# Optimization experiments

Hardware: AMD Instinct MI355X
Metric: run time of the kernel (lower is better)

## Reference

```python
import jax, jax.numpy as jnp
import numpy as np

N_EVENTS = 4_000_000
T_WINDOW = 100.0


def setup_inputs() -> dict:
    key = jax.random.key(0)
    k_ts, = jax.random.split(key, 1)
    # sorted event times in [0, T)
    ts = jnp.sort(jax.random.uniform(k_ts, (N_EVENTS,), dtype=jnp.float32) * T_WINDOW)
    mu = jnp.float32(0.5)
    log_alpha = jnp.log(jnp.float32(0.5))   # alpha = 0.5 (branching ratio < 1)
    log_beta = jnp.log(jnp.float32(2.0))    # beta = 2.0
    return {"ts": ts, "mu": mu, "log_alpha": log_alpha, "log_beta": log_beta, "T": 100}


def reference(ts, mu, log_alpha, log_beta, T):
    """Log-likelihood of a univariate exponential-kernel Hawkes process.

    Equivalent to UnivariateHawkesProcess.likelihood(ts, T, log=True,
    num_integration_points=0, analy_kernel=True), but the O(N^2) per-event
    Python loop is replaced by a stable O(N) exclusive cumulative logsumexp:
        sum_{j<i} exp(-beta (t_i - t_j)) = exp(logcumsumexp(beta t)_{i-1} - beta t_i)
    """
    alpha = jnp.exp(log_alpha)
    beta = jnp.exp(log_beta)
    Tf = jnp.asarray(T, dtype=ts.dtype)

    b_ts = beta * ts                               # [N]
    incl = jax.lax.cumlogsumexp(b_ts)              # inclusive running logsumexp
    excl = jnp.concatenate([jnp.full((1,), -jnp.inf, dtype=b_ts.dtype), incl[:-1]])
    decay_sum = jnp.exp(excl - b_ts)               # sum_{j<i} exp(-beta(t_i - t_j))
    intensities = mu + alpha * beta * decay_sum    # lambda(t_i | history)
    positive_ll = jnp.sum(jnp.log(intensities))

    # analytic compensator: mu*T + sum_i alpha/beta * (1 - exp(-beta (T - t_i)))
    integral = mu * Tf + jnp.sum((alpha / beta) * (1.0 - jnp.exp(-beta * (Tf - ts))))
    return positive_ll - integral
```

## Files before the change

### kernel.cpp

```cpp
#include <hip/hip_runtime.h>

#define SEG 64
#define TPB 256

struct DA { float d, a; };

__device__ __forceinline__ DA da_compose(DA f, DA g) {
    DA r; r.d = f.d * g.d; r.a = fmaf(f.a, g.d, g.a); return r;
}

__global__ void __launch_bounds__(TPB) hawkes_phase1(
    const float* __restrict__ ts, const float* __restrict__ lb_p,
    const int* __restrict__ T_p, int N, int NSEG,
    DA* __restrict__ segDA, DA* __restrict__ blkDA)
{
    const float beta = __expf(*lb_p);
    const int tid = threadIdx.x;
    const int g = blockIdx.x * TPB + tid;

    DA my; my.d = 1.f; my.a = 0.f;
    if (g < NSEG) {
        const int start = g * SEG;
        const int end = min(start + SEG, N);
        const float Tf = (float)(*T_p);
        const float rnext = (end < N) ? ts[end] : Tf;
        float R, t0, tprev;
        if (end == start + SEG) {
            const float4* p = (const float4*)(ts + start);
            float4 v = p[0];
            t0 = v.x; tprev = t0; R = 1.f;
            { float e = __expf(-beta * (v.y - tprev)); R = fmaf(R, e, 1.f); tprev = v.y; }
            { float e = __expf(-beta * (v.z - tprev)); R = fmaf(R, e, 1.f); tprev = v.z; }
            { float e = __expf(-beta * (v.w - tprev)); R = fmaf(R, e, 1.f); tprev = v.w; }
            #pragma unroll
            for (int q = 1; q < SEG / 4; ++q) {
                float4 w4 = p[q];
                { float e = __expf(-beta * (w4.x - tprev)); R = fmaf(R, e, 1.f); tprev = w4.x; }
                { float e = __expf(-beta * (w4.y - tprev)); R = fmaf(R, e, 1.f); tprev = w4.y; }
                { float e = __expf(-beta * (w4.z - tprev)); R = fmaf(R, e, 1.f); tprev = w4.z; }
                { float e = __expf(-beta * (w4.w - tprev)); R = fmaf(R, e, 1.f); tprev = w4.w; }
            }
        } else {
            t0 = ts[start]; tprev = t0; R = 1.f;
            for (int j = start + 1; j < end; ++j) {
                float t = ts[j];
                float e = __expf(-beta * (t - tprev)); R = fmaf(R, e, 1.f); tprev = t;
            }
        }
        my.a = R * __expf(-beta * (rnext - tprev));
        my.d = __expf(-beta * (rnext - t0));
        segDA[g] = my;
    }

    __shared__ DA lds[TPB];
    lds[tid] = my;
    __syncthreads();
    #pragma unroll
    for (int s = 1; s < TPB; s <<= 1) {
        if ((tid & (2 * s - 1)) == 0) lds[tid] = da_compose(lds[tid], lds[tid + s]);
        __syncthreads();
    }
    if (tid == 0) blkDA[blockIdx.x] = lds[0];
}

__global__ void __launch_bounds__(TPB) hawkes_phase2(
    const DA* __restrict__ blkDA, int NB,
    float* __restrict__ blkCarry, float* __restrict__ stats ,
    double* __restrict__ acc)
{
    const int tid = threadIdx.x;
    if (tid == 0) *acc = 0.0;

    const int K2 = (NB + TPB - 1) / TPB;
    const int b0 = min(tid * K2, NB);
    const int b1 = min(b0 + K2, NB);

    DA comp; comp.d = 1.f; comp.a = 0.f;
    for (int b = b0; b < b1; ++b) comp = da_compose(comp, blkDA[b]);

    const int lane = tid & 63, wave = tid >> 6;
    DA inc = comp;
    #pragma unroll
    for (int off = 1; off < 64; off <<= 1) {
        DA up; up.d = __shfl_up(inc.d, off); up.a = __shfl_up(inc.a, off);
        if (lane >= off) inc = da_compose(up, inc);
    }
    __shared__ DA waveAgg[TPB / 64];
    if (lane == 63) waveAgg[wave] = inc;
    __syncthreads();
    DA pre; pre.d = 1.f; pre.a = 0.f;
    for (int w = 0; w < wave; ++w) pre = da_compose(pre, waveAgg[w]);
    DA lexcl; lexcl.d = __shfl_up(inc.d, 1); lexcl.a = __shfl_up(inc.a, 1);
    if (lane == 0) { lexcl.d = 1.f; lexcl.a = 0.f; }
    DA excl = da_compose(pre, lexcl);

    float c = excl.a;
    for (int b = b0; b < b1; ++b) {
        blkCarry[b] = c;
        DA x = blkDA[b];
        c = fmaf(c, x.d, x.a);
    }
    if (b0 < NB && b1 == NB) stats[0] = c;
}

__global__ void __launch_bounds__(TPB) hawkes_phase3(
    const float* __restrict__ ts,
    const float* __restrict__ mu_p, const float* __restrict__ la_p,
    const float* __restrict__ lb_p, int N, int NSEG,
    const DA* __restrict__ segDA, const float* __restrict__ blkCarry,
    double* __restrict__ acc)
{
    const float mu = *mu_p;
    const float beta = __expf(*lb_p);
    const float ab = __expf(*la_p) * beta;
    const int tid = threadIdx.x;
    const int g = blockIdx.x * TPB + tid;
    const int lane = tid & 63, wave = tid >> 6;

    DA my; my.d = 1.f; my.a = 0.f;
    if (g < NSEG) my = segDA[g];

    DA inc = my;
    #pragma unroll
    for (int off = 1; off < 64; off <<= 1) {
        DA up; up.d = __shfl_up(inc.d, off); up.a = __shfl_up(inc.a, off);
        if (lane >= off) inc = da_compose(up, inc);
    }
    __shared__ DA waveAgg[TPB / 64];
    if (lane == 63) waveAgg[wave] = inc;
    __syncthreads();
    DA pre; pre.d = 1.f; pre.a = 0.f;
    for (int w = 0; w < wave; ++w) pre = da_compose(pre, waveAgg[w]);
    DA lexcl; lexcl.d = __shfl_up(inc.d, 1); lexcl.a = __shfl_up(inc.a, 1);
    if (lane == 0) { lexcl.d = 1.f; lexcl.a = 0.f; }
    DA excl = da_compose(pre, lexcl);

    const float bc = blkCarry[blockIdx.x];
    float S = fmaf(bc, excl.d, excl.a);

    float lsum = 0.f;
    if (g < NSEG) {
        const int start = g * SEG;
        const int end = min(start + SEG, N);
        if (end == start + SEG) {
            const float4* p = (const float4*)(ts + start);
            float4 v = p[0];
            float tprev = v.x;
            lsum += __logf(fmaf(ab, S, mu));
#define HSTEP(tt) { float e = __expf(-beta * ((tt) - tprev)); S = fmaf(S, e, e); \
                    lsum += __logf(fmaf(ab, S, mu)); tprev = (tt); }
            HSTEP(v.y); HSTEP(v.z); HSTEP(v.w);
            #pragma unroll
            for (int q = 1; q < SEG / 4; ++q) {
                float4 w4 = p[q];
                HSTEP(w4.x); HSTEP(w4.y); HSTEP(w4.z); HSTEP(w4.w);
            }
#undef HSTEP
        } else {
            float tprev = ts[start];
            lsum += __logf(fmaf(ab, S, mu));
            for (int j = start + 1; j < end; ++j) {
                float t = ts[j];
                float e = __expf(-beta * (t - tprev));
                S = fmaf(S, e, e);
                lsum += __logf(fmaf(ab, S, mu));
                tprev = t;
            }
        }
    }

    #pragma unroll
    for (int off = 32; off > 0; off >>= 1) lsum += __shfl_down(lsum, off);
    __shared__ float wsum[TPB / 64];
    if (lane == 0) wsum[wave] = lsum;
    __syncthreads();
    if (tid == 0) {
        float tot = 0.f;
        #pragma unroll
        for (int w = 0; w < TPB / 64; ++w) tot += wsum[w];
        atomicAdd(acc, (double)tot);
    }
}

__global__ void hawkes_phase4(
    const double* __restrict__ acc, const float* __restrict__ stats,
    const float* __restrict__ mu_p, const float* __restrict__ la_p,
    const float* __restrict__ lb_p, const int* __restrict__ T_p,
    int N, float* __restrict__ out)
{
    const float mu = *mu_p;
    const float alpha = __expf(*la_p);
    const float beta = __expf(*lb_p);
    const float Tf = (float)(*T_p);
    const float integral = mu * Tf + (alpha / beta) * ((float)N - stats[0]);
    out[0] = (float)(*acc) - integral;
}

extern "C" void kernel_launch(void* const* d_in, const int* in_sizes, int n_in,
                              void* d_out, int out_size, void* d_ws, size_t ws_size,
                              hipStream_t stream) {
    const float* ts = (const float*)d_in[0];
    const float* mu = (const float*)d_in[1];
    const float* la = (const float*)d_in[2];
    const float* lb = (const float*)d_in[3];
    const int*   T  = (const int*)d_in[4];
    const int N = in_sizes[0];
    const int NSEG = (N + SEG - 1) / SEG;
    const int NB = (NSEG + TPB - 1) / TPB;

    char* w = (char*)d_ws;
    double* acc      = (double*)w;
    float*  stats    = (float*)(w + 8);
    DA*     segDA    = (DA*)(w + 16);
    DA*     blkDA    = (DA*)(w + 16 + (size_t)NSEG * sizeof(DA));
    float*  blkCarry = (float*)(w + 16 + (size_t)(NSEG + NB) * sizeof(DA));

    hawkes_phase1<<<NB, TPB, 0, stream>>>(ts, lb, T, N, NSEG, segDA, blkDA);
    hawkes_phase2<<<1, TPB, 0, stream>>>(blkDA, NB, blkCarry, stats, acc);
    hawkes_phase3<<<NB, TPB, 0, stream>>>(ts, mu, la, lb, N, NSEG, segDA, blkCarry, acc);
    hawkes_phase4<<<1, 1, 0, stream>>>(acc, stats, mu, la, lb, T, N, (float*)d_out);
}
```

Before: 82.33 us.

## Fuse four scan phases into one cooperative kernel with register-cached decays

Replaces the four-kernel pipeline (segment aggregate, block-carry scan, local rescan, finalize) with a single cooperative kernel that uses grid-wide syncs between phases. Each thread keeps its 64 decay factors in registers, so the second pass needs neither the re-read of ts nor the exp recompute, and segDA no longer goes to global memory. The global atomic is replaced by per-block partial sums that block 0 reduces at the end. The design relies on all NB blocks (about 245 here) being co-resident for the grid sync. It also adds register pressure from the 64-float array and the cost of grid barriers.

```diff
diff --git a/kernel.cpp b/kernel.cpp
--- a/kernel.cpp
+++ b/kernel.cpp
@@ -1,4 +1,7 @@
 #include <hip/hip_runtime.h>
+#include <hip/hip_cooperative_groups.h>
+
+namespace cg = cooperative_groups;
 
 #define SEG 64
 #define TPB 256
@@ -9,77 +12,69 @@
     DA r; r.d = f.d * g.d; r.a = fmaf(f.a, g.d, g.a); return r;
 }
 
-__global__ void __launch_bounds__(TPB) hawkes_phase1(
-    const float* __restrict__ ts, const float* __restrict__ lb_p,
-    const int* __restrict__ T_p, int N, int NSEG,
-    DA* __restrict__ segDA, DA* __restrict__ blkDA)
+__global__ void __launch_bounds__(TPB, 1) hawkes_fused(
+    const float* __restrict__ ts,
+    const float* __restrict__ mu_p, const float* __restrict__ la_p,
+    const float* __restrict__ lb_p, const int* __restrict__ T_p,
+    int N, int NSEG, int NB,
+    DA* __restrict__ blkDA, float* __restrict__ blkCarry,
+    double* __restrict__ blkSum, float* __restrict__ stats,
+    float* __restrict__ out)
 {
-    const float beta = __expf(*lb_p);
-    const int tid = threadIdx.x;
-    const int g = blockIdx.x * TPB + tid;
-
+    cg::grid_group grid = cg::this_grid();
+    const float beta  = __expf(*lb_p);
+    const float mu    = *mu_p;
+    const float alpha = __expf(*la_p);
+    const float ab    = alpha * beta;
+    const float Tf    = (float)(*T_p);
+    const int tid  = threadIdx.x;
+    const int g    = blockIdx.x * TPB + tid;
+    const int lane = tid & 63, wave = tid >> 6;
+
+    float e[SEG];
     DA my; my.d = 1.f; my.a = 0.f;
+    bool full = false;
+    const int start = g * SEG;
+    const int end   = (g < NSEG) ? min(start + SEG, N) : start;
     if (g < NSEG) {
-        const int start = g * SEG;
-        const int end = min(start + SEG, N);
-        const float Tf = (float)(*T_p);
+        full = (end == start + SEG);
         const float rnext = (end < N) ? ts[end] : Tf;
-        float R, t0, tprev;
-        if (end == start + SEG) {
+        float R = 1.f, t0, tprev;
+        if (full) {
             const float4* p = (const float4*)(ts + start);
             float4 v = p[0];
-            t0 = v.x; tprev = t0; R = 1.f;
-            { float e = __expf(-beta * (v.y - tprev)); R = fmaf(R, e, 1.f); tprev = v.y; }
-            { float e = __expf(-beta * (v.z - tprev)); R = fmaf(R, e, 1.f); tprev = v.z; }
-            { float e = __expf(-beta * (v.w - tprev)); R = fmaf(R, e, 1.f); tprev = v.w; }
+            t0 = v.x;
+            e[1] = __expf(-beta * (v.y - v.x));
+            e[2] = __expf(-beta * (v.z - v.y));
+            e[3] = __expf(-beta * (v.w - v.z));
+            R = fmaf(R, e[1], 1.f); R = fmaf(R, e[2], 1.f); R = fmaf(R, e[3], 1.f);
+            tprev = v.w;
             #pragma unroll
             for (int q = 1; q < SEG / 4; ++q) {
                 float4 w4 = p[q];
-                { float e = __expf(-beta * (w4.x - tprev)); R = fmaf(R, e, 1.f); tprev = w4.x; }
-                { float e = __expf(-beta * (w4.y - tprev)); R = fmaf(R, e, 1.f); tprev = w4.y; }
-                { float e = __expf(-beta * (w4.z - tprev)); R = fmaf(R, e, 1.f); tprev = w4.z; }
-                { float e = __expf(-beta * (w4.w - tprev)); R = fmaf(R, e, 1.f); tprev = w4.w; }
+                e[4*q+0] = __expf(-beta * (w4.x - tprev));
+                e[4*q+1] = __expf(-beta * (w4.y - w4.x));
+                e[4*q+2] = __expf(-beta * (w4.z - w4.y));
+                e[4*q+3] = __expf(-beta * (w4.w - w4.z));
+                R = fmaf(R, e[4*q+0], 1.f);
+                R = fmaf(R, e[4*q+1], 1.f);
+                R = fmaf(R, e[4*q+2], 1.f);
+                R = fmaf(R, e[4*q+3], 1.f);
+                tprev = w4.w;
             }
         } else {
-            t0 = ts[start]; tprev = t0; R = 1.f;
+            t0 = ts[start]; tprev = t0;
             for (int j = start + 1; j < end; ++j) {
                 float t = ts[j];
-                float e = __expf(-beta * (t - tprev)); R = fmaf(R, e, 1.f); tprev = t;
+                float ee = __expf(-beta * (t - tprev));
+                R = fmaf(R, ee, 1.f); tprev = t;
             }
         }
         my.a = R * __expf(-beta * (rnext - tprev));
         my.d = __expf(-beta * (rnext - t0));
-        segDA[g] = my;
-    }
-
-    __shared__ DA lds[TPB];
-    lds[tid] = my;
-    __syncthreads();
-    #pragma unroll
-    for (int s = 1; s < TPB; s <<= 1) {
-        if ((tid & (2 * s - 1)) == 0) lds[tid] = da_compose(lds[tid], lds[tid + s]);
-        __syncthreads();
-    }
-    if (tid == 0) blkDA[blockIdx.x] = lds[0];
-}
-
-__global__ void __launch_bounds__(TPB) hawkes_phase2(
-    const DA* __restrict__ blkDA, int NB,
-    float* __restrict__ blkCarry, float* __restrict__ stats ,
-    double* __restrict__ acc)
-{
-    const int tid = threadIdx.x;
-    if (tid == 0) *acc = 0.0;
-
-    const int K2 = (NB + TPB - 1) / TPB;
-    const int b0 = min(tid * K2, NB);
-    const int b1 = min(b0 + K2, NB);
-
-    DA comp; comp.d = 1.f; comp.a = 0.f;
-    for (int b = b0; b < b1; ++b) comp = da_compose(comp, blkDA[b]);
-
-    const int lane = tid & 63, wave = tid >> 6;
-    DA inc = comp;
+    }
+
+    DA inc = my;
     #pragma unroll
     for (int off = 1; off < 64; off <<= 1) {
         DA up; up.d = __shfl_up(inc.d, off); up.a = __shfl_up(inc.a, off);
@@ -93,82 +88,69 @@
     DA lexcl; lexcl.d = __shfl_up(inc.d, 1); lexcl.a = __shfl_up(inc.a, 1);
     if (lane == 0) { lexcl.d = 1.f; lexcl.a = 0.f; }
     DA excl = da_compose(pre, lexcl);
-
-    float c = excl.a;
-    for (int b = b0; b < b1; ++b) {
-        blkCarry[b] = c;
-        DA x = blkDA[b];
-        c = fmaf(c, x.d, x.a);
-    }
-    if (b0 < NB && b1 == NB) stats[0] = c;
-}
-
-__global__ void __launch_bounds__(TPB) hawkes_phase3(
-    const float* __restrict__ ts,
-    const float* __restrict__ mu_p, const float* __restrict__ la_p,
-    const float* __restrict__ lb_p, int N, int NSEG,
-    const DA* __restrict__ segDA, const float* __restrict__ blkCarry,
-    double* __restrict__ acc)
-{
-    const float mu = *mu_p;
-    const float beta = __expf(*lb_p);
-    const float ab = __expf(*la_p) * beta;
-    const int tid = threadIdx.x;
-    const int g = blockIdx.x * TPB + tid;
-    const int lane = tid & 63, wave = tid >> 6;
-
-    DA my; my.d = 1.f; my.a = 0.f;
-    if (g < NSEG) my = segDA[g];
-
-    DA inc = my;
-    #pragma unroll
-    for (int off = 1; off < 64; off <<= 1) {
-        DA up; up.d = __shfl_up(inc.d, off); up.a = __shfl_up(inc.a, off);
-        if (lane >= off) inc = da_compose(up, inc);
-    }
-    __shared__ DA waveAgg[TPB / 64];
-    if (lane == 63) waveAgg[wave] = inc;
-    __syncthreads();
-    DA pre; pre.d = 1.f; pre.a = 0.f;
-    for (int w = 0; w < wave; ++w) pre = da_compose(pre, waveAgg[w]);
-    DA lexcl; lexcl.d = __shfl_up(inc.d, 1); lexcl.a = __shfl_up(inc.a, 1);
-    if (lane == 0) { lexcl.d = 1.f; lexcl.a = 0.f; }
-    DA excl = da_compose(pre, lexcl);
+    if (tid == TPB - 1) {
+        DA agg = da_compose(pre, inc);
+        blkDA[blockIdx.x] = agg;
+    }
+    __threadfence();
+    grid.sync();
+
+    if (blockIdx.x == 0) {
+        const int K2 = (NB + TPB - 1) / TPB;
+        const int b0 = min(tid * K2, NB);
+        const int b1 = min(b0 + K2, NB);
+        DA comp; comp.d = 1.f; comp.a = 0.f;
+        for (int b = b0; b < b1; ++b) comp = da_compose(comp, blkDA[b]);
+        DA inc2 = comp;
+        #pragma unroll
+        for (int off = 1; off < 64; off <<= 1) {
+            DA up; up.d = __shfl_up(inc2.d, off); up.a = __shfl_up(inc2.a, off);
+            if (lane >= off) inc2 = da_compose(up, inc2);
+        }
+        __shared__ DA waveAgg2[TPB / 64];
+        if (lane == 63) waveAgg2[wave] = inc2;
+        __syncthreads();
+        DA pre2; pre2.d = 1.f; pre2.a = 0.f;
+        for (int w = 0; w < wave; ++w) pre2 = da_compose(pre2, waveAgg2[w]);
+        DA lex2; lex2.d = __shfl_up(inc2.d, 1); lex2.a = __shfl_up(inc2.a, 1);
+        if (lane == 0) { lex2.d = 1.f; lex2.a = 0.f; }
+        DA ex2 = da_compose(pre2, lex2);
+        float c = ex2.a;
+        for (int b = b0; b < b1; ++b) {
+            blkCarry[b] = c;
+            DA x = blkDA[b];
+            c = fmaf(c, x.d, x.a);
+        }
+        if (b0 < NB && b1 == NB) stats[0] = c;
+        __threadfence();
+    }
+    grid.sync();
 
     const float bc = blkCarry[blockIdx.x];
     float S = fmaf(bc, excl.d, excl.a);
-
-    float lsum = 0.f;
+    float lsum0 = 0.f, lsum1 = 0.f;
     if (g < NSEG) {
-        const int start = g * SEG;
-        const int end = min(start + SEG, N);
-        if (end == start + SEG) {
-            const float4* p = (const float4*)(ts + start);
-            float4 v = p[0];
-            float tprev = v.x;
-            lsum += __logf(fmaf(ab, S, mu));
-#define HSTEP(tt) { float e = __expf(-beta * ((tt) - tprev)); S = fmaf(S, e, e); \
-                    lsum += __logf(fmaf(ab, S, mu)); tprev = (tt); }
-            HSTEP(v.y); HSTEP(v.z); HSTEP(v.w);
+        if (full) {
+            lsum0 += __logf(fmaf(ab, S, mu));
             #pragma unroll
-            for (int q = 1; q < SEG / 4; ++q) {
-                float4 w4 = p[q];
-                HSTEP(w4.x); HSTEP(w4.y); HSTEP(w4.z); HSTEP(w4.w);
-            }
-#undef HSTEP
+            for (int k = 1; k < SEG - 1; k += 2) {
+                { float ek = e[k];   S = fmaf(S, ek, ek); lsum1 += __logf(fmaf(ab, S, mu)); }
+                { float ek = e[k+1]; S = fmaf(S, ek, ek); lsum0 += __logf(fmaf(ab, S, mu)); }
+            }
+            { float ek = e[SEG-1]; S = fmaf(S, ek, ek); lsum1 += __logf(fmaf(ab, S, mu)); }
         } else {
             float tprev = ts[start];
-            lsum += __logf(fmaf(ab, S, mu));
+            lsum0 += __logf(fmaf(ab, S, mu));
             for (int j = start + 1; j < end; ++j) {
                 float t = ts[j];
-                float e = __expf(-beta * (t - tprev));
-                S = fmaf(S, e, e);
-                lsum += __logf(fmaf(ab, S, mu));
+                float ee = __expf(-beta * (t - tprev));
+                S = fmaf(S, ee, ee);
+                lsum0 += __logf(fmaf(ab, S, mu));
                 tprev = t;
             }
         }
     }
-
+    float lsum = lsum0 + lsum1;
     #pragma unroll
     for (int off = 32; off > 0; off >>= 1) lsum += __shfl_down(lsum, off);
     __shared__ float wsum[TPB / 64];
@@ -178,22 +160,26 @@
         float tot = 0.f;
         #pragma unroll
         for (int w = 0; w < TPB / 64; ++w) tot += wsum[w];
-        atomicAdd(acc, (double)tot);
-    }
-}
-
-__global__ void hawkes_phase4(
-    const double* __restrict__ acc, const float* __restrict__ stats,
-    const float* __restrict__ mu_p, const float* __restrict__ la_p,
-    const float* __restrict__ lb_p, const int* __restrict__ T_p,
-    int N, float* __restrict__ out)
-{
-    const float mu = *mu_p;
-    const float alpha = __expf(*la_p);
-    const float beta = __expf(*lb_p);
-    const float Tf = (float)(*T_p);
-    const float integral = mu * Tf + (alpha / beta) * ((float)N - stats[0]);
-    out[0] = (float)(*acc) - integral;
+        blkSum[blockIdx.x] = (double)tot;
+    }
+    __threadfence();
+    grid.sync();
+
+    if (blockIdx.x == 0) {
+        double v = (tid < NB) ? blkSum[tid] : 0.0;
+        #pragma unroll
+        for (int off = 32; off > 0; off >>= 1) v += __shfl_down(v, off);
+        __shared__ double dsum[TPB / 64];
+        if (lane == 0) dsum[wave] = v;
+        __syncthreads();
+        if (tid == 0) {
+            double tot = 0.0;
+            #pragma unroll
+            for (int w = 0; w < TPB / 64; ++w) tot += dsum[w];
+            const float integral = mu * Tf + (alpha / beta) * ((float)N - stats[0]);
+            out[0] = (float)(tot - (double)integral);
+        }
+    }
 }
 
 extern "C" void kernel_launch(void* const* d_in, const int* in_sizes, int n_in,
@@ -204,19 +190,21 @@
     const float* la = (const float*)d_in[2];
     const float* lb = (const float*)d_in[3];
     const int*   T  = (const int*)d_in[4];
-    const int N = in_sizes[0];
-    const int NSEG = (N + SEG - 1) / SEG;
-    const int NB = (NSEG + TPB - 1) / TPB;
+    int N = in_sizes[0];
+    int NSEG = (N + SEG - 1) / SEG;
+    int NB = (NSEG + TPB - 1) / TPB;
 
     char* w = (char*)d_ws;
-    double* acc      = (double*)w;
-    float*  stats    = (float*)(w + 8);
-    DA*     segDA    = (DA*)(w + 16);
-    DA*     blkDA    = (DA*)(w + 16 + (size_t)NSEG * sizeof(DA));
-    float*  blkCarry = (float*)(w + 16 + (size_t)(NSEG + NB) * sizeof(DA));
-
-    hawkes_phase1<<<NB, TPB, 0, stream>>>(ts, lb, T, N, NSEG, segDA, blkDA);
-    hawkes_phase2<<<1, TPB, 0, stream>>>(blkDA, NB, blkCarry, stats, acc);
-    hawkes_phase3<<<NB, TPB, 0, stream>>>(ts, mu, la, lb, N, NSEG, segDA, blkCarry, acc);
-    hawkes_phase4<<<1, 1, 0, stream>>>(acc, stats, mu, la, lb, T, N, (float*)d_out);
+    double* blkSum   = (double*)w;
+    DA*     blkDA    = (DA*)(w + (size_t)NB * 8);
+    float*  blkCarry = (float*)(w + (size_t)NB * 16);
+    float*  stats    = (float*)(w + (size_t)NB * 20);
+    float*  out      = (float*)d_out;
+
+    void* args[] = { (void*)&ts, (void*)&mu, (void*)&la, (void*)&lb, (void*)&T,
+                     (void*)&N, (void*)&NSEG, (void*)&NB,
+                     (void*)&blkDA, (void*)&blkCarry, (void*)&blkSum,
+                     (void*)&stats, (void*)&out };
+    hipLaunchCooperativeKernel((const void*)hawkes_fused, dim3(NB), dim3(TPB),
+                               args, 0, stream);
 }
```

New measurement: 202.5 us. 146% more time.

## Fuse four-phase scan into two kernels with redundant block-carry scan and ticket finish

Applied to the files above, without the earlier changes.

Reduces the pipeline from four launches to two. Each block in the second kernel redundantly scans all block aggregates to get its own carry, and the last block to arrive (via an atomic ticket) writes the final result. The per-segment DA array is dropped, and the second kernel recomputes segment summaries from ts, keeping the exponentials in registers. The segment length falls from 64 to 16, giving four times more blocks for occupancy. In exchange, the exp work is duplicated across both kernels and every block rereads the full block-aggregate array.

```diff
diff --git a/kernel.cpp b/kernel.cpp
--- a/kernel.cpp
+++ b/kernel.cpp
@@ -1,6 +1,6 @@
 #include <hip/hip_runtime.h>
 
-#define SEG 64
+#define SEG 16
 #define TPB 256
 
 struct DA { float d, a; };
@@ -9,160 +9,191 @@
     DA r; r.d = f.d * g.d; r.a = fmaf(f.a, g.d, g.a); return r;
 }
 
-__global__ void __launch_bounds__(TPB) hawkes_phase1(
+__global__ void __launch_bounds__(TPB) hawkes_k1(
     const float* __restrict__ ts, const float* __restrict__ lb_p,
     const int* __restrict__ T_p, int N, int NSEG,
-    DA* __restrict__ segDA, DA* __restrict__ blkDA)
+    DA* __restrict__ blkDA, double* __restrict__ acc, unsigned* __restrict__ ticket)
 {
     const float beta = __expf(*lb_p);
+    const float Tf = (float)(*T_p);
     const int tid = threadIdx.x;
     const int g = blockIdx.x * TPB + tid;
+    const int lane = tid & 63, wave = tid >> 6;
+
+    if (blockIdx.x == 0 && tid == 0) { *acc = 0.0; *ticket = 0u; }
 
     DA my; my.d = 1.f; my.a = 0.f;
     if (g < NSEG) {
         const int start = g * SEG;
         const int end = min(start + SEG, N);
-        const float Tf = (float)(*T_p);
-        const float rnext = (end < N) ? ts[end] : Tf;
-        float R, t0, tprev;
+        float R = 1.f, t0, tlast;
         if (end == start + SEG) {
             const float4* p = (const float4*)(ts + start);
-            float4 v = p[0];
-            t0 = v.x; tprev = t0; R = 1.f;
-            { float e = __expf(-beta * (v.y - tprev)); R = fmaf(R, e, 1.f); tprev = v.y; }
-            { float e = __expf(-beta * (v.z - tprev)); R = fmaf(R, e, 1.f); tprev = v.z; }
-            { float e = __expf(-beta * (v.w - tprev)); R = fmaf(R, e, 1.f); tprev = v.w; }
-            #pragma unroll
-            for (int q = 1; q < SEG / 4; ++q) {
-                float4 w4 = p[q];
-                { float e = __expf(-beta * (w4.x - tprev)); R = fmaf(R, e, 1.f); tprev = w4.x; }
-                { float e = __expf(-beta * (w4.y - tprev)); R = fmaf(R, e, 1.f); tprev = w4.y; }
-                { float e = __expf(-beta * (w4.z - tprev)); R = fmaf(R, e, 1.f); tprev = w4.z; }
-                { float e = __expf(-beta * (w4.w - tprev)); R = fmaf(R, e, 1.f); tprev = w4.w; }
-            }
+            float4 a = p[0], b = p[1], c = p[2], d = p[3];
+            t0 = a.x;
+            float tp = a.x;
+#define K1S(tt) { R = fmaf(R, __expf(-beta * ((tt) - tp)), 1.f); tp = (tt); }
+            K1S(a.y) K1S(a.z) K1S(a.w)
+            K1S(b.x) K1S(b.y) K1S(b.z) K1S(b.w)
+            K1S(c.x) K1S(c.y) K1S(c.z) K1S(c.w)
+            K1S(d.x) K1S(d.y) K1S(d.z) K1S(d.w)
+#undef K1S
+            tlast = d.w;
         } else {
-            t0 = ts[start]; tprev = t0; R = 1.f;
+            t0 = ts[start]; tlast = t0;
             for (int j = start + 1; j < end; ++j) {
                 float t = ts[j];
-                float e = __expf(-beta * (t - tprev)); R = fmaf(R, e, 1.f); tprev = t;
-            }
-        }
-        my.a = R * __expf(-beta * (rnext - tprev));
+                R = fmaf(R, __expf(-beta * (t - tlast)), 1.f); tlast = t;
+            }
+        }
+        const float rnext = (end < N) ? ts[end] : Tf;
+        my.a = R * __expf(-beta * (rnext - tlast));
         my.d = __expf(-beta * (rnext - t0));
-        segDA[g] = my;
-    }
-
-    __shared__ DA lds[TPB];
-    lds[tid] = my;
-    __syncthreads();
-    #pragma unroll
-    for (int s = 1; s < TPB; s <<= 1) {
-        if ((tid & (2 * s - 1)) == 0) lds[tid] = da_compose(lds[tid], lds[tid + s]);
-        __syncthreads();
-    }
-    if (tid == 0) blkDA[blockIdx.x] = lds[0];
-}
-
-__global__ void __launch_bounds__(TPB) hawkes_phase2(
-    const DA* __restrict__ blkDA, int NB,
-    float* __restrict__ blkCarry, float* __restrict__ stats ,
-    double* __restrict__ acc)
-{
-    const int tid = threadIdx.x;
-    if (tid == 0) *acc = 0.0;
-
-    const int K2 = (NB + TPB - 1) / TPB;
-    const int b0 = min(tid * K2, NB);
-    const int b1 = min(b0 + K2, NB);
-
-    DA comp; comp.d = 1.f; comp.a = 0.f;
-    for (int b = b0; b < b1; ++b) comp = da_compose(comp, blkDA[b]);
-
-    const int lane = tid & 63, wave = tid >> 6;
-    DA inc = comp;
+    }
+
+    DA inc = my;
     #pragma unroll
     for (int off = 1; off < 64; off <<= 1) {
         DA up; up.d = __shfl_up(inc.d, off); up.a = __shfl_up(inc.a, off);
         if (lane >= off) inc = da_compose(up, inc);
     }
-    __shared__ DA waveAgg[TPB / 64];
-    if (lane == 63) waveAgg[wave] = inc;
+    __shared__ DA wagg[TPB / 64];
+    if (lane == 63) wagg[wave] = inc;
+    __syncthreads();
+    if (tid == 0) {
+        DA aggr = wagg[0];
+        #pragma unroll
+        for (int w = 1; w < TPB / 64; ++w) aggr = da_compose(aggr, wagg[w]);
+        blkDA[blockIdx.x] = aggr;
+    }
+}
+
+__global__ void __launch_bounds__(TPB) hawkes_k2(
+    const float* __restrict__ ts,
+    const float* __restrict__ mu_p, const float* __restrict__ la_p,
+    const float* __restrict__ lb_p, const int* __restrict__ T_p,
+    int N, int NSEG, int NB,
+    const DA* __restrict__ blkDA, double* __restrict__ acc,
+    unsigned* __restrict__ ticket, float* __restrict__ out)
+{
+    const float beta  = __expf(*lb_p);
+    const float mu    = *mu_p;
+    const float alpha = __expf(*la_p);
+    const float ab    = alpha * beta;
+    const float Tf    = (float)(*T_p);
+    const int tid = threadIdx.x;
+    const int g = blockIdx.x * TPB + tid;
+    const int lane = tid & 63, wave = tid >> 6;
+
+    float e[SEG];
+    DA my; my.d = 1.f; my.a = 0.f;
+    bool full = false;
+    const int start = g * SEG;
+    const int end = (g < NSEG) ? min(start + SEG, N) : start;
+    if (g < NSEG) {
+        full = (end == start + SEG);
+        float R = 1.f, t0, tlast;
+        if (full) {
+            const float4* p = (const float4*)(ts + start);
+            float4 a = p[0], b = p[1], c = p[2], d = p[3];
+            t0 = a.x;
+            e[1]  = __expf(-beta * (a.y - a.x));
+            e[2]  = __expf(-beta * (a.z - a.y));
+            e[3]  = __expf(-beta * (a.w - a.z));
+            e[4]  = __expf(-beta * (b.x - a.w));
+            e[5]  = __expf(-beta * (b.y - b.x));
+            e[6]  = __expf(-beta * (b.z - b.y));
+            e[7]  = __expf(-beta * (b.w - b.z));
+            e[8]  = __expf(-beta * (c.x - b.w));
+            e[9]  = __expf(-beta * (c.y - c.x));
+            e[10] = __expf(-beta * (c.z - c.y));
+            e[11] = __expf(-beta * (c.w - c.z));
+            e[12] = __expf(-beta * (d.x - c.w));
+            e[13] = __expf(-beta * (d.y - d.x));
+            e[14] = __expf(-beta * (d.z - d.y));
+            e[15] = __expf(-beta * (d.w - d.z));
+            #pragma unroll
+            for (int k = 1; k < SEG; ++k) R = fmaf(R, e[k], 1.f);
+            tlast = d.w;
+        } else {
+            t0 = ts[start]; tlast = t0;
+            for (int j = start + 1; j < end; ++j) {
+                float t = ts[j];
+                R = fmaf(R, __expf(-beta * (t - tlast)), 1.f); tlast = t;
+            }
+        }
+        const float rnext = (end < N) ? ts[end] : Tf;
+        my.a = R * __expf(-beta * (rnext - tlast));
+        my.d = __expf(-beta * (rnext - t0));
+    }
+
+    DA inc = my;
+    #pragma unroll
+    for (int off = 1; off < 64; off <<= 1) {
+        DA up; up.d = __shfl_up(inc.d, off); up.a = __shfl_up(inc.a, off);
+        if (lane >= off) inc = da_compose(up, inc);
+    }
+    __shared__ DA wagg[TPB / 64];
+    if (lane == 63) wagg[wave] = inc;
     __syncthreads();
     DA pre; pre.d = 1.f; pre.a = 0.f;
-    for (int w = 0; w < wave; ++w) pre = da_compose(pre, waveAgg[w]);
+    for (int w = 0; w < wave; ++w) pre = da_compose(pre, wagg[w]);
     DA lexcl; lexcl.d = __shfl_up(inc.d, 1); lexcl.a = __shfl_up(inc.a, 1);
     if (lane == 0) { lexcl.d = 1.f; lexcl.a = 0.f; }
     DA excl = da_compose(pre, lexcl);
 
-    float c = excl.a;
-    for (int b = b0; b < b1; ++b) {
-        blkCarry[b] = c;
-        DA x = blkDA[b];
-        c = fmaf(c, x.d, x.a);
-    }
-    if (b0 < NB && b1 == NB) stats[0] = c;
-}
-
-__global__ void __launch_bounds__(TPB) hawkes_phase3(
-    const float* __restrict__ ts,
-    const float* __restrict__ mu_p, const float* __restrict__ la_p,
-    const float* __restrict__ lb_p, int N, int NSEG,
-    const DA* __restrict__ segDA, const float* __restrict__ blkCarry,
-    double* __restrict__ acc)
-{
-    const float mu = *mu_p;
-    const float beta = __expf(*lb_p);
-    const float ab = __expf(*la_p) * beta;
-    const int tid = threadIdx.x;
-    const int g = blockIdx.x * TPB + tid;
-    const int lane = tid & 63, wave = tid >> 6;
-
-    DA my; my.d = 1.f; my.a = 0.f;
-    if (g < NSEG) my = segDA[g];
-
-    DA inc = my;
+    const int CH = (NB + TPB - 1) / TPB;
+    DA comp; comp.d = 1.f; comp.a = 0.f;
+    for (int j = 0; j < CH; ++j) {
+        const int idx = tid * CH + j;
+        if (idx < NB) comp = da_compose(comp, blkDA[idx]);
+    }
+    DA inc2 = comp;
     #pragma unroll
     for (int off = 1; off < 64; off <<= 1) {
-        DA up; up.d = __shfl_up(inc.d, off); up.a = __shfl_up(inc.a, off);
-        if (lane >= off) inc = da_compose(up, inc);
-    }
-    __shared__ DA waveAgg[TPB / 64];
-    if (lane == 63) waveAgg[wave] = inc;
-    __syncthreads();
-    DA pre; pre.d = 1.f; pre.a = 0.f;
-    for (int w = 0; w < wave; ++w) pre = da_compose(pre, waveAgg[w]);
-    DA lexcl; lexcl.d = __shfl_up(inc.d, 1); lexcl.a = __shfl_up(inc.a, 1);
-    if (lane == 0) { lexcl.d = 1.f; lexcl.a = 0.f; }
-    DA excl = da_compose(pre, lexcl);
-
-    const float bc = blkCarry[blockIdx.x];
-    float S = fmaf(bc, excl.d, excl.a);
-
+        DA up; up.d = __shfl_up(inc2.d, off); up.a = __shfl_up(inc2.a, off);
+        if (lane >= off) inc2 = da_compose(up, inc2);
+    }
+    __shared__ DA wagg2[TPB / 64];
+    if (lane == 63) wagg2[wave] = inc2;
+    __syncthreads();
+    DA pre2; pre2.d = 1.f; pre2.a = 0.f;
+    for (int w = 0; w < wave; ++w) pre2 = da_compose(pre2, wagg2[w]);
+    DA lex2; lex2.d = __shfl_up(inc2.d, 1); lex2.a = __shfl_up(inc2.a, 1);
+    if (lane == 0) { lex2.d = 1.f; lex2.a = 0.f; }
+    DA chunkExcl = da_compose(pre2, lex2);
+
+    __shared__ DA exclArr[TPB];
+    __shared__ DA totalSh;
+    exclArr[tid] = chunkExcl;
+    if (tid == TPB - 1) totalSh = da_compose(pre2, inc2);
+    __syncthreads();
+
+    const int b = blockIdx.x;
+    const int c0 = b / CH, pp = b - c0 * CH;
+    DA E = exclArr[c0];
+    for (int j = 0; j < pp; ++j) E = da_compose(E, blkDA[c0 * CH + j]);
+    const float carry = E.a;
+    const float S_T = totalSh.a;
+
+    float S = fmaf(carry, excl.d, excl.a);
     float lsum = 0.f;
     if (g < NSEG) {
-        const int start = g * SEG;
-        const int end = min(start + SEG, N);
-        if (end == start + SEG) {
-            const float4* p = (const float4*)(ts + start);
-            float4 v = p[0];
-            float tprev = v.x;
+        if (full) {
             lsum += __logf(fmaf(ab, S, mu));
-#define HSTEP(tt) { float e = __expf(-beta * ((tt) - tprev)); S = fmaf(S, e, e); \
-                    lsum += __logf(fmaf(ab, S, mu)); tprev = (tt); }
-            HSTEP(v.y); HSTEP(v.z); HSTEP(v.w);
             #pragma unroll
-            for (int q = 1; q < SEG / 4; ++q) {
-                float4 w4 = p[q];
-                HSTEP(w4.x); HSTEP(w4.y); HSTEP(w4.z); HSTEP(w4.w);
-            }
-#undef HSTEP
+            for (int k = 1; k < SEG; ++k) {
+                float ek = e[k];
+                S = fmaf(S, ek, ek);
+                lsum += __logf(fmaf(ab, S, mu));
+            }
         } else {
             float tprev = ts[start];
             lsum += __logf(fmaf(ab, S, mu));
             for (int j = start + 1; j < end; ++j) {
                 float t = ts[j];
-                float e = __expf(-beta * (t - tprev));
-                S = fmaf(S, e, e);
+                float ee = __expf(-beta * (t - tprev));
+                S = fmaf(S, ee, ee);
                 lsum += __logf(fmaf(ab, S, mu));
                 tprev = t;
             }
@@ -179,21 +210,15 @@
         #pragma unroll
         for (int w = 0; w < TPB / 64; ++w) tot += wsum[w];
         atomicAdd(acc, (double)tot);
-    }
-}
-
-__global__ void hawkes_phase4(
-    const double* __restrict__ acc, const float* __restrict__ stats,
-    const float* __restrict__ mu_p, const float* __restrict__ la_p,
-    const float* __restrict__ lb_p, const int* __restrict__ T_p,
-    int N, float* __restrict__ out)
-{
-    const float mu = *mu_p;
-    const float alpha = __expf(*la_p);
-    const float beta = __expf(*lb_p);
-    const float Tf = (float)(*T_p);
-    const float integral = mu * Tf + (alpha / beta) * ((float)N - stats[0]);
-    out[0] = (float)(*acc) - integral;
+        __threadfence();
+        unsigned old = atomicAdd(ticket, 1u);
+        if (old == (unsigned)(NB - 1)) {
+            __threadfence();
+            double tt = atomicAdd(acc, 0.0);
+            const float integral = mu * Tf + (alpha / beta) * ((float)N - S_T);
+            out[0] = (float)(tt - (double)integral);
+        }
+    }
 }
 
 extern "C" void kernel_launch(void* const* d_in, const int* in_sizes, int n_in,
@@ -209,14 +234,11 @@
     const int NB = (NSEG + TPB - 1) / TPB;
 
     char* w = (char*)d_ws;
-    double* acc      = (double*)w;
-    float*  stats    = (float*)(w + 8);
-    DA*     segDA    = (DA*)(w + 16);
-    DA*     blkDA    = (DA*)(w + 16 + (size_t)NSEG * sizeof(DA));
-    float*  blkCarry = (float*)(w + 16 + (size_t)(NSEG + NB) * sizeof(DA));
-
-    hawkes_phase1<<<NB, TPB, 0, stream>>>(ts, lb, T, N, NSEG, segDA, blkDA);
-    hawkes_phase2<<<1, TPB, 0, stream>>>(blkDA, NB, blkCarry, stats, acc);
-    hawkes_phase3<<<NB, TPB, 0, stream>>>(ts, mu, la, lb, N, NSEG, segDA, blkCarry, acc);
-    hawkes_phase4<<<1, 1, 0, stream>>>(acc, stats, mu, la, lb, T, N, (float*)d_out);
-}
+    double*   acc    = (double*)w;
+    unsigned* ticket = (unsigned*)(w + 8);
+    DA*       blkDA  = (DA*)(w + 16);
+
+    hawkes_k1<<<NB, TPB, 0, stream>>>(ts, lb, T, N, NSEG, blkDA, acc, ticket);
+    hawkes_k2<<<NB, TPB, 0, stream>>>(ts, mu, la, lb, T, N, NSEG, NB, blkDA, acc, ticket,
+                                      (float*)d_out);
+}
```

After: 100.1 us. 21.6% more time.

## Fuse block-carry scan and finalization into main pass using ticket counter

Applied to the files above, without the earlier changes.

Replaces the four-kernel pipeline with two kernels. Each block of the second kernel redundantly scans the block aggregates to get its own carry, and the last block to draw a ticket writes the final result. This removes the single-block scan launch and the finalization launch. Log accumulation is also split across two accumulators to shorten the dependency chain. The carry scan assumes the number of blocks fits in one thread block.

```diff
diff --git a/kernel.cpp b/kernel.cpp
--- a/kernel.cpp
+++ b/kernel.cpp
@@ -9,26 +9,28 @@
     DA r; r.d = f.d * g.d; r.a = fmaf(f.a, g.d, g.a); return r;
 }
 
-__global__ void __launch_bounds__(TPB) hawkes_phase1(
+__global__ void __launch_bounds__(TPB) hawkes_k1(
     const float* __restrict__ ts, const float* __restrict__ lb_p,
     const int* __restrict__ T_p, int N, int NSEG,
-    DA* __restrict__ segDA, DA* __restrict__ blkDA)
+    DA* __restrict__ segDA, DA* __restrict__ blkDA,
+    double* __restrict__ acc, unsigned* __restrict__ ticket)
 {
     const float beta = __expf(*lb_p);
     const int tid = threadIdx.x;
     const int g = blockIdx.x * TPB + tid;
+
+    if (blockIdx.x == 0 && tid == 0) { *acc = 0.0; *ticket = 0u; }
 
     DA my; my.d = 1.f; my.a = 0.f;
     if (g < NSEG) {
         const int start = g * SEG;
         const int end = min(start + SEG, N);
         const float Tf = (float)(*T_p);
-        const float rnext = (end < N) ? ts[end] : Tf;
-        float R, t0, tprev;
+        float R = 1.f, t0, tprev;
         if (end == start + SEG) {
             const float4* p = (const float4*)(ts + start);
             float4 v = p[0];
-            t0 = v.x; tprev = t0; R = 1.f;
+            t0 = v.x; tprev = v.x;
             { float e = __expf(-beta * (v.y - tprev)); R = fmaf(R, e, 1.f); tprev = v.y; }
             { float e = __expf(-beta * (v.z - tprev)); R = fmaf(R, e, 1.f); tprev = v.z; }
             { float e = __expf(-beta * (v.w - tprev)); R = fmaf(R, e, 1.f); tprev = v.w; }
@@ -41,12 +43,13 @@
                 { float e = __expf(-beta * (w4.w - tprev)); R = fmaf(R, e, 1.f); tprev = w4.w; }
             }
         } else {
-            t0 = ts[start]; tprev = t0; R = 1.f;
+            t0 = ts[start]; tprev = t0;
             for (int j = start + 1; j < end; ++j) {
                 float t = ts[j];
                 float e = __expf(-beta * (t - tprev)); R = fmaf(R, e, 1.f); tprev = t;
             }
         }
+        const float rnext = (end < N) ? ts[end] : Tf;
         my.a = R * __expf(-beta * (rnext - tprev));
         my.d = __expf(-beta * (rnext - t0));
         segDA[g] = my;
@@ -63,82 +66,70 @@
     if (tid == 0) blkDA[blockIdx.x] = lds[0];
 }
 
-__global__ void __launch_bounds__(TPB) hawkes_phase2(
-    const DA* __restrict__ blkDA, int NB,
-    float* __restrict__ blkCarry, float* __restrict__ stats ,
-    double* __restrict__ acc)
+__global__ void __launch_bounds__(TPB) hawkes_k2(
+    const float* __restrict__ ts,
+    const float* __restrict__ mu_p, const float* __restrict__ la_p,
+    const float* __restrict__ lb_p, const int* __restrict__ T_p,
+    int N, int NSEG, int NB,
+    const DA* __restrict__ segDA, const DA* __restrict__ blkDA,
+    double* __restrict__ acc, unsigned* __restrict__ ticket,
+    float* __restrict__ out)
 {
-    const int tid = threadIdx.x;
-    if (tid == 0) *acc = 0.0;
-
-    const int K2 = (NB + TPB - 1) / TPB;
-    const int b0 = min(tid * K2, NB);
-    const int b1 = min(b0 + K2, NB);
-
-    DA comp; comp.d = 1.f; comp.a = 0.f;
-    for (int b = b0; b < b1; ++b) comp = da_compose(comp, blkDA[b]);
-
+    const float beta  = __expf(*lb_p);
+    const float mu    = *mu_p;
+    const float alpha = __expf(*la_p);
+    const float ab    = alpha * beta;
+    const float Tf    = (float)(*T_p);
+    const int tid  = threadIdx.x;
+    const int g    = blockIdx.x * TPB + tid;
     const int lane = tid & 63, wave = tid >> 6;
-    DA inc = comp;
+
+    __shared__ DA wagg[TPB / 64];
+    __shared__ DA bwagg[TPB / 64];
+    __shared__ float carrySh, stSh;
+    __shared__ float wsum[TPB / 64];
+
+    DA my; my.d = 1.f; my.a = 0.f;
+    if (g < NSEG) my = segDA[g];
+    DA inc = my;
     #pragma unroll
     for (int off = 1; off < 64; off <<= 1) {
         DA up; up.d = __shfl_up(inc.d, off); up.a = __shfl_up(inc.a, off);
         if (lane >= off) inc = da_compose(up, inc);
     }
-    __shared__ DA waveAgg[TPB / 64];
-    if (lane == 63) waveAgg[wave] = inc;
+    if (lane == 63) wagg[wave] = inc;
     __syncthreads();
     DA pre; pre.d = 1.f; pre.a = 0.f;
-    for (int w = 0; w < wave; ++w) pre = da_compose(pre, waveAgg[w]);
+    for (int w = 0; w < wave; ++w) pre = da_compose(pre, wagg[w]);
     DA lexcl; lexcl.d = __shfl_up(inc.d, 1); lexcl.a = __shfl_up(inc.a, 1);
     if (lane == 0) { lexcl.d = 1.f; lexcl.a = 0.f; }
     DA excl = da_compose(pre, lexcl);
 
-    float c = excl.a;
-    for (int b = b0; b < b1; ++b) {
-        blkCarry[b] = c;
-        DA x = blkDA[b];
-        c = fmaf(c, x.d, x.a);
-    }
-    if (b0 < NB && b1 == NB) stats[0] = c;
-}
-
-__global__ void __launch_bounds__(TPB) hawkes_phase3(
-    const float* __restrict__ ts,
-    const float* __restrict__ mu_p, const float* __restrict__ la_p,
-    const float* __restrict__ lb_p, int N, int NSEG,
-    const DA* __restrict__ segDA, const float* __restrict__ blkCarry,
-    double* __restrict__ acc)
-{
-    const float mu = *mu_p;
-    const float beta = __expf(*lb_p);
-    const float ab = __expf(*la_p) * beta;
-    const int tid = threadIdx.x;
-    const int g = blockIdx.x * TPB + tid;
-    const int lane = tid & 63, wave = tid >> 6;
-
-    DA my; my.d = 1.f; my.a = 0.f;
-    if (g < NSEG) my = segDA[g];
-
-    DA inc = my;
+    DA bval; bval.d = 1.f; bval.a = 0.f;
+    if (tid < NB) bval = blkDA[tid];
+    DA binc = bval;
     #pragma unroll
     for (int off = 1; off < 64; off <<= 1) {
-        DA up; up.d = __shfl_up(inc.d, off); up.a = __shfl_up(inc.a, off);
-        if (lane >= off) inc = da_compose(up, inc);
-    }
-    __shared__ DA waveAgg[TPB / 64];
-    if (lane == 63) waveAgg[wave] = inc;
-    __syncthreads();
-    DA pre; pre.d = 1.f; pre.a = 0.f;
-    for (int w = 0; w < wave; ++w) pre = da_compose(pre, waveAgg[w]);
-    DA lexcl; lexcl.d = __shfl_up(inc.d, 1); lexcl.a = __shfl_up(inc.a, 1);
-    if (lane == 0) { lexcl.d = 1.f; lexcl.a = 0.f; }
-    DA excl = da_compose(pre, lexcl);
-
-    const float bc = blkCarry[blockIdx.x];
+        DA up; up.d = __shfl_up(binc.d, off); up.a = __shfl_up(binc.a, off);
+        if (lane >= off) binc = da_compose(up, binc);
+    }
+    if (lane == 63) bwagg[wave] = binc;
+    __syncthreads();
+    DA bpre; bpre.d = 1.f; bpre.a = 0.f;
+    for (int w = 0; w < wave; ++w) bpre = da_compose(bpre, bwagg[w]);
+    DA blex; blex.d = __shfl_up(binc.d, 1); blex.a = __shfl_up(binc.a, 1);
+    if (lane == 0) { blex.d = 1.f; blex.a = 0.f; }
+    DA bexcl = da_compose(bpre, blex);
+    if (tid == blockIdx.x) carrySh = bexcl.a;
+    if (tid == NB - 1) {
+        DA full = da_compose(bpre, binc);
+        stSh = full.a;
+    }
+    __syncthreads();
+
+    const float bc = carrySh;
     float S = fmaf(bc, excl.d, excl.a);
-
-    float lsum = 0.f;
+    float lsum0 = 0.f, lsum1 = 0.f;
     if (g < NSEG) {
         const int start = g * SEG;
         const int end = min(start + SEG, N);
@@ -146,54 +137,55 @@
             const float4* p = (const float4*)(ts + start);
             float4 v = p[0];
             float tprev = v.x;
-            lsum += __logf(fmaf(ab, S, mu));
-#define HSTEP(tt) { float e = __expf(-beta * ((tt) - tprev)); S = fmaf(S, e, e); \
-                    lsum += __logf(fmaf(ab, S, mu)); tprev = (tt); }
-            HSTEP(v.y); HSTEP(v.z); HSTEP(v.w);
+            lsum0 += __logf(fmaf(ab, S, mu));
+#define HSTEP0(tt) { float e = __expf(-beta * ((tt) - tprev)); S = fmaf(S, e, e); \
+                     lsum0 += __logf(fmaf(ab, S, mu)); tprev = (tt); }
+#define HSTEP1(tt) { float e = __expf(-beta * ((tt) - tprev)); S = fmaf(S, e, e); \
+                     lsum1 += __logf(fmaf(ab, S, mu)); tprev = (tt); }
+            HSTEP1(v.y); HSTEP0(v.z); HSTEP1(v.w);
             #pragma unroll
             for (int q = 1; q < SEG / 4; ++q) {
                 float4 w4 = p[q];
-                HSTEP(w4.x); HSTEP(w4.y); HSTEP(w4.z); HSTEP(w4.w);
-            }
-#undef HSTEP
+                HSTEP0(w4.x); HSTEP1(w4.y); HSTEP0(w4.z); HSTEP1(w4.w);
+            }
+#undef HSTEP0
+#undef HSTEP1
         } else {
             float tprev = ts[start];
-            lsum += __logf(fmaf(ab, S, mu));
+            lsum0 += __logf(fmaf(ab, S, mu));
             for (int j = start + 1; j < end; ++j) {
                 float t = ts[j];
                 float e = __expf(-beta * (t - tprev));
                 S = fmaf(S, e, e);
-                lsum += __logf(fmaf(ab, S, mu));
+                lsum0 += __logf(fmaf(ab, S, mu));
                 tprev = t;
             }
         }
     }
+    float lsum = lsum0 + lsum1;
 
     #pragma unroll
     for (int off = 32; off > 0; off >>= 1) lsum += __shfl_down(lsum, off);
-    __shared__ float wsum[TPB / 64];
     if (lane == 0) wsum[wave] = lsum;
     __syncthreads();
     if (tid == 0) {
         float tot = 0.f;
         #pragma unroll
         for (int w = 0; w < TPB / 64; ++w) tot += wsum[w];
-        atomicAdd(acc, (double)tot);
-    }
-}
-
-__global__ void hawkes_phase4(
-    const double* __restrict__ acc, const float* __restrict__ stats,
-    const float* __restrict__ mu_p, const float* __restrict__ la_p,
-    const float* __restrict__ lb_p, const int* __restrict__ T_p,
-    int N, float* __restrict__ out)
-{
-    const float mu = *mu_p;
-    const float alpha = __expf(*la_p);
-    const float beta = __expf(*lb_p);
-    const float Tf = (float)(*T_p);
-    const float integral = mu * Tf + (alpha / beta) * ((float)N - stats[0]);
-    out[0] = (float)(*acc) - integral;
+        double add = (double)tot;
+        if (blockIdx.x == NB - 1) {
+            const float integral = mu * Tf + (alpha / beta) * ((float)N - stSh);
+            add -= (double)integral;
+        }
+        atomicAdd(acc, add);
+        __threadfence();
+        unsigned old = atomicAdd(ticket, 1u);
+        if (old == (unsigned)(NB - 1)) {
+            __threadfence();
+            double tt = atomicAdd(acc, 0.0);
+            out[0] = (float)tt;
+        }
+    }
 }
 
 extern "C" void kernel_launch(void* const* d_in, const int* in_sizes, int n_in,
@@ -209,14 +201,12 @@
     const int NB = (NSEG + TPB - 1) / TPB;
 
     char* w = (char*)d_ws;
-    double* acc      = (double*)w;
-    float*  stats    = (float*)(w + 8);
-    DA*     segDA    = (DA*)(w + 16);
-    DA*     blkDA    = (DA*)(w + 16 + (size_t)NSEG * sizeof(DA));
-    float*  blkCarry = (float*)(w + 16 + (size_t)(NSEG + NB) * sizeof(DA));
-
-    hawkes_phase1<<<NB, TPB, 0, stream>>>(ts, lb, T, N, NSEG, segDA, blkDA);
-    hawkes_phase2<<<1, TPB, 0, stream>>>(blkDA, NB, blkCarry, stats, acc);
-    hawkes_phase3<<<NB, TPB, 0, stream>>>(ts, mu, la, lb, N, NSEG, segDA, blkCarry, acc);
-    hawkes_phase4<<<1, 1, 0, stream>>>(acc, stats, mu, la, lb, T, N, (float*)d_out);
-}
+    double*   acc    = (double*)w;
+    unsigned* ticket = (unsigned*)(w + 8);
+    DA*       blkDA  = (DA*)(w + 16);
+    DA*       segDA  = (DA*)(w + 16 + (size_t)NB * 8);
+
+    hawkes_k1<<<NB, TPB, 0, stream>>>(ts, lb, T, N, NSEG, segDA, blkDA, acc, ticket);
+    hawkes_k2<<<NB, TPB, 0, stream>>>(ts, mu, la, lb, T, N, NSEG, NB,
+                                      segDA, blkDA, acc, ticket, (float*)d_out);
+}
```

New measurement: 83.32 us. No clear change (+1.2%).
